# Optimization experiments

Measured on AMD Instinct MI355X. Metric: run time of the kernel, lower is better.

Reference implementation:

```python
import jax, jax.numpy as jnp
import numpy as np

N_NODES = 200000
N_GRAPHS = 64
K_SLOTS = 16
LATENT = 128
HID = 128  # hidden_dim // 2


def setup_inputs() -> dict:
    key = jax.random.key(0)
    ks = jax.random.split(key, 8)
    z = jax.random.normal(ks[0], (N_GRAPHS, K_SLOTS, LATENT), dtype=jnp.float32)
    s = jax.random.uniform(ks[1], (N_NODES, K_SLOTS), dtype=jnp.float32)
    batch = jnp.sort(jax.random.randint(ks[2], (N_NODES,), 0, N_GRAPHS))
    sc1 = 1.0 / np.sqrt(LATENT)
    sc2 = 1.0 / np.sqrt(HID)
    W1 = jax.random.normal(ks[3], (LATENT, HID), dtype=jnp.float32) * sc1
    b1 = jnp.zeros((HID,), dtype=jnp.float32)
    W2 = jax.random.normal(ks[4], (HID, HID), dtype=jnp.float32) * sc2
    b2 = jnp.zeros((HID,), dtype=jnp.float32)
    Wp = jax.random.normal(ks[5], (HID, 2), dtype=jnp.float32) * sc2
    bp = jnp.zeros((2,), dtype=jnp.float32)
    Wv = jax.random.normal(ks[6], (HID, 2), dtype=jnp.float32) * sc2
    bv = jnp.zeros((2,), dtype=jnp.float32)
    return {"z": z, "s": s, "batch": batch, "W1": W1, "b1": b1,
            "W2": W2, "b2": b2, "Wp": Wp, "bp": bp, "Wv": Wv, "bv": bv}


def reference(z, s, batch, W1, b1, W2, b2, Wp, bp, Wv, bv):
    # gather per-node latent set: [N, K, D]
    z_expanded = z[batch]
    # weighted sum over K slots -> [N, D]
    node_feat = jnp.einsum('nk,nkd->nd', s, z_expanded)
    # shared MLP: Linear-ReLU-Linear-ReLU
    h = jax.nn.relu(node_feat @ W1 + b1)
    h = jax.nn.relu(h @ W2 + b2)
    # heads
    pos_recon = jnp.tanh(h @ Wp + bp)
    vel_recon = h @ Wv + bv
    return jnp.concatenate([pos_recon, vel_recon], axis=-1)
```

## Files before the change

kernel.cpp:

```cpp
#include <hip/hip_runtime.h>

typedef _Float16 half4 __attribute__((ext_vector_type(4)));
typedef float    f32x4 __attribute__((ext_vector_type(4)));

#define MFMA16(a,b,c) __builtin_amdgcn_mfma_f32_16x16x16f16((a),(b),(c),0,0,0)

static constexpr int N_NODES  = 200000;
static constexpr int N_GRAPHS = 64;
static constexpr int GPG      = 256;
static constexpr int TOTAL_G  = N_GRAPHS * GPG;

static constexpr size_t WS_ZWT    = 0;
static constexpr size_t WS_W2T    = 262144;
static constexpr size_t WS_WHT    = 294912;
static constexpr size_t WS_GSTART = 299008;

__global__ __launch_bounds__(256) void gnn_prep(
    const int* __restrict__ batch,
    const float* __restrict__ z,
    const float* __restrict__ W1,
    const float* __restrict__ W2,
    const float* __restrict__ Wp,
    const float* __restrict__ Wv,
    int* __restrict__ gstart,
    _Float16* __restrict__ zwt,
    _Float16* __restrict__ w2t,
    _Float16* __restrict__ wht)
{
    const int b = blockIdx.x, t = threadIdx.x;
    if (b < 782) {
        const int i = b * 256 + t;
        if (i < N_NODES) {
            const int bi   = batch[i];
            const int prev = (i == 0) ? -1 : batch[i - 1];
            if (bi != prev)
                for (int g = prev + 1; g <= bi; ++g) gstart[g] = i;
            if (i == N_NODES - 1)
                for (int g = bi + 1; g <= N_GRAPHS; ++g) gstart[g] = N_NODES;
        }
    } else if (b < 846) {
        const int e = (b - 782) * 256 + t;
        const int n = e >> 7, kk = e & 127;
        w2t[e] = (_Float16)W2[kk * 128 + n];
    } else if (b < 854) {
        const int e = (b - 846) * 256 + t;
        const int j = e >> 7, d = e & 127;
        float v = 0.f;
        if (j < 2)      v = Wp[d * 2 + j];
        else if (j < 4) v = Wv[d * 2 + (j - 2)];
        wht[e] = (_Float16)v;
    } else {
        const int p = (b - 854) * 2 + (t >> 7);
        const int g = p >> 4, k = p & 15, d = t & 127;
        const float* zr = z + (g * 16 + k) * 128;
        float a0 = 0.f, a1 = 0.f, a2 = 0.f, a3 = 0.f;
#pragma unroll 8
        for (int c = 0; c < 128; c += 4) {
            a0 += zr[c    ] * W1[(c    ) * 128 + d];
            a1 += zr[c + 1] * W1[(c + 1) * 128 + d];
            a2 += zr[c + 2] * W1[(c + 2) * 128 + d];
            a3 += zr[c + 3] * W1[(c + 3) * 128 + d];
        }
        zwt[(g * 128 + d) * 16 + k] = (_Float16)((a0 + a1) + (a2 + a3));
    }
}

__device__ inline float fast_tanh(float x) {
    x = fminf(fmaxf(x, -15.f), 15.f);
    const float e = __expf(2.f * x);
    return (e - 1.f) / (e + 1.f);
}

__global__ __launch_bounds__(256, 2) void gnn_main(
    const float* __restrict__ s,
    const float* __restrict__ b1,
    const float* __restrict__ b2,
    const float* __restrict__ bp,
    const float* __restrict__ bv,
    const _Float16* __restrict__ zwt,
    const _Float16* __restrict__ w2t,
    const _Float16* __restrict__ wht,
    const int* __restrict__ gstart,
    float* __restrict__ out)
{
    const int lane = threadIdx.x & 63;
    const int n16  = lane & 15;
    const int quad = lane >> 4;
    const int wid  = blockIdx.x * 4 + (threadIdx.x >> 6);
    const int nw   = gridDim.x * 4;

    half4 a2[8][8];
#pragma unroll
    for (int mt = 0; mt < 8; ++mt)
#pragma unroll
        for (int t = 0; t < 8; ++t)
            a2[mt][t] = *(const half4*)(w2t + (mt * 16 + n16) * 128 + t * 16 + quad * 4);

    half4 a3[8];
#pragma unroll
    for (int t = 0; t < 8; ++t)
        a3[t] = *(const half4*)(wht + n16 * 128 + t * 16 + quad * 4);

    const float bp0 = bp[0], bp1 = bp[1], bv0 = bv[0], bv1 = bv[1];

    for (int gi = wid; gi < TOTAL_G; gi += nw) {
        const int g    = gi >> 8;
        const int idx  = gi & 255;
        const int gs   = gstart[g];
        const int ge   = gstart[g + 1];
        const int base = gs + idx * 16;
        if (base >= ge) continue;

        const int node  = base + n16;
        const bool valid = node < ge;

        half4 bs = {(_Float16)0.f, (_Float16)0.f, (_Float16)0.f, (_Float16)0.f};
        if (valid) {
            const f32x4 sv = *(const f32x4*)(s + node * 16 + quad * 4);
            bs[0] = (_Float16)sv[0]; bs[1] = (_Float16)sv[1];
            bs[2] = (_Float16)sv[2]; bs[3] = (_Float16)sv[3];
        }

        const _Float16* zg = zwt + g * 2048;
        half4 h1[8];
#pragma unroll
        for (int mt = 0; mt < 8; ++mt) {
            const half4 a1 = *(const half4*)(zg + (mt * 16 + n16) * 16 + quad * 4);
            const f32x4 zc = {0.f, 0.f, 0.f, 0.f};
            const f32x4 acc = MFMA16(a1, bs, zc);
            const f32x4 bb = *(const f32x4*)(b1 + mt * 16 + quad * 4);
#pragma unroll
            for (int i = 0; i < 4; ++i)
                h1[mt][i] = (_Float16)fmaxf(acc[i] + bb[i], 0.f);
        }

        f32x4 acc3 = {0.f, 0.f, 0.f, 0.f};
#pragma unroll
        for (int mo = 0; mo < 8; ++mo) {
            f32x4 acc2 = {0.f, 0.f, 0.f, 0.f};
#pragma unroll
            for (int t = 0; t < 8; ++t)
                acc2 = MFMA16(a2[mo][t], h1[t], acc2);
            const f32x4 bb = *(const f32x4*)(b2 + mo * 16 + quad * 4);
            half4 h2;
#pragma unroll
            for (int i = 0; i < 4; ++i)
                h2[i] = (_Float16)fmaxf(acc2[i] + bb[i], 0.f);
            acc3 = MFMA16(a3[mo], h2, acc3);
        }

        if (quad == 0 && valid) {
            f32x4 o;
            o[0] = fast_tanh(acc3[0] + bp0);
            o[1] = fast_tanh(acc3[1] + bp1);
            o[2] = acc3[2] + bv0;
            o[3] = acc3[3] + bv1;
            *(f32x4*)(out + node * 4) = o;
        }
    }
}

extern "C" void kernel_launch(void* const* d_in, const int* in_sizes, int n_in,
                              void* d_out, int out_size, void* d_ws, size_t ws_size,
                              hipStream_t stream)
{
    const float* z     = (const float*)d_in[0];
    const float* s     = (const float*)d_in[1];
    const int*   batch = (const int*)d_in[2];
    const float* W1    = (const float*)d_in[3];
    const float* b1    = (const float*)d_in[4];
    const float* W2    = (const float*)d_in[5];
    const float* b2    = (const float*)d_in[6];
    const float* Wp    = (const float*)d_in[7];
    const float* bp    = (const float*)d_in[8];
    const float* Wv    = (const float*)d_in[9];
    const float* bv    = (const float*)d_in[10];
    float* out = (float*)d_out;

    char* w = (char*)d_ws;
    _Float16* zwt = (_Float16*)(w + WS_ZWT);
    _Float16* w2t = (_Float16*)(w + WS_W2T);
    _Float16* wht = (_Float16*)(w + WS_WHT);
    int* gstart   = (int*)(w + WS_GSTART);

    hipLaunchKernelGGL(gnn_prep, dim3(1366), dim3(256), 0, stream,
                       batch, z, W1, W2, Wp, Wv, gstart, zwt, w2t, wht);
    hipLaunchKernelGGL(gnn_main, dim3(512), dim3(256), 0, stream,
                       s, b1, b2, bp, bv, zwt, w2t, wht, gstart, out);
}
```

Measured before the change: 126.9 us.

## Stage MLP weights in LDS, process two node tiles per wave, raise occupancy

W2 and head weights move out of per-thread registers (64 half4 per lane) into shared memory, packed as half8, with the biases staged there too. This frees registers so launch bounds can go to 4 blocks per SM and the grid doubles to 1024 blocks. Each wave now handles 32 nodes as two 16-node MFMA tiles that share each weight fetch, which amortizes LDS reads. Biases are folded into the MFMA accumulator init. The cost is LDS bandwidth and a prologue copy in every block.

```diff
diff --git a/kernel.cpp b/kernel.cpp
--- a/kernel.cpp
+++ b/kernel.cpp
@@ -1,19 +1,21 @@
 #include <hip/hip_runtime.h>
 
 typedef _Float16 half4 __attribute__((ext_vector_type(4)));
+typedef _Float16 half8 __attribute__((ext_vector_type(8)));
 typedef float    f32x4 __attribute__((ext_vector_type(4)));
 
 #define MFMA16(a,b,c) __builtin_amdgcn_mfma_f32_16x16x16f16((a),(b),(c),0,0,0)
 
 static constexpr int N_NODES  = 200000;
 static constexpr int N_GRAPHS = 64;
-static constexpr int GPG      = 256;
-static constexpr int TOTAL_G  = N_GRAPHS * GPG;
+static constexpr int SGPG     = 128;
+static constexpr int TOTAL_SG = N_GRAPHS * SGPG;
 
 static constexpr size_t WS_ZWT    = 0;
 static constexpr size_t WS_W2T    = 262144;
 static constexpr size_t WS_WHT    = 294912;
 static constexpr size_t WS_GSTART = 299008;
+
 
 __global__ __launch_bounds__(256) void gnn_prep(
     const int* __restrict__ batch,
@@ -71,7 +73,7 @@
     return (e - 1.f) / (e + 1.f);
 }
 
-__global__ __launch_bounds__(256, 2) void gnn_main(
+__global__ __launch_bounds__(256, 4) void gnn_main(
     const float* __restrict__ s,
     const float* __restrict__ b1,
     const float* __restrict__ b2,
@@ -83,79 +85,129 @@
     const int* __restrict__ gstart,
     float* __restrict__ out)
 {
-    const int lane = threadIdx.x & 63;
+    __shared__ char lds[37888];
+    half8* a2l = (half8*)lds;
+    half4* a3l = (half4*)(lds + 32768);
+    float* b1l = (float*)(lds + 36864);
+    float* b2l = (float*)(lds + 37376);
+
+    const int tid  = threadIdx.x;
+    const int lane = tid & 63;
     const int n16  = lane & 15;
     const int quad = lane >> 4;
-    const int wid  = blockIdx.x * 4 + (threadIdx.x >> 6);
-    const int nw   = gridDim.x * 4;
-
-    half4 a2[8][8];
-#pragma unroll
-    for (int mt = 0; mt < 8; ++mt)
-#pragma unroll
-        for (int t = 0; t < 8; ++t)
-            a2[mt][t] = *(const half4*)(w2t + (mt * 16 + n16) * 128 + t * 16 + quad * 4);
-
-    half4 a3[8];
-#pragma unroll
-    for (int t = 0; t < 8; ++t)
-        a3[t] = *(const half4*)(wht + n16 * 128 + t * 16 + quad * 4);
+
+#pragma unroll
+    for (int r = 0; r < 8; ++r) {
+        const int e  = r * 256 + tid;
+        const int mo = e >> 8, tp = (e >> 6) & 3, ll = e & 63;
+        const int nn = ll & 15, qq = ll >> 4;
+        const _Float16* srcp = w2t + (mo * 16 + nn) * 128 + tp * 32 + qq * 4;
+        half8 v;
+        *(half4*)&v     = *(const half4*)srcp;
+        *((half4*)&v+1) = *(const half4*)(srcp + 16);
+        a2l[e] = v;
+    }
+    {
+        const int e = tid;
+#pragma unroll
+        for (int r = 0; r < 2; ++r) {
+            const int ee = r * 256 + e;
+            const int tt = ee >> 6, ll = ee & 63;
+            const int nn = ll & 15, qq = ll >> 4;
+            a3l[ee] = *(const half4*)(wht + nn * 128 + tt * 16 + qq * 4);
+        }
+        if (tid < 128)      b1l[tid] = b1[tid];
+        else                b2l[tid - 128] = b2[tid - 128];
+    }
+    __syncthreads();
 
     const float bp0 = bp[0], bp1 = bp[1], bv0 = bv[0], bv1 = bv[1];
-
-    for (int gi = wid; gi < TOTAL_G; gi += nw) {
-        const int g    = gi >> 8;
-        const int idx  = gi & 255;
+    f32x4 c3init = {0.f, 0.f, 0.f, 0.f};
+    if (quad == 0) { c3init[0] = bp0; c3init[1] = bp1; c3init[2] = bv0; c3init[3] = bv1; }
+
+    const int wid = blockIdx.x * 4 + (tid >> 6);
+    const int nw  = gridDim.x * 4;
+
+    for (int sgi = wid; sgi < TOTAL_SG; sgi += nw) {
+        const int g    = sgi >> 7;
+        const int idx  = sgi & 127;
         const int gs   = gstart[g];
         const int ge   = gstart[g + 1];
-        const int base = gs + idx * 16;
+        const int base = gs + idx * 32;
         if (base >= ge) continue;
 
-        const int node  = base + n16;
-        const bool valid = node < ge;
-
-        half4 bs = {(_Float16)0.f, (_Float16)0.f, (_Float16)0.f, (_Float16)0.f};
-        if (valid) {
-            const f32x4 sv = *(const f32x4*)(s + node * 16 + quad * 4);
-            bs[0] = (_Float16)sv[0]; bs[1] = (_Float16)sv[1];
-            bs[2] = (_Float16)sv[2]; bs[3] = (_Float16)sv[3];
+        const int nodeA = base + n16;
+        const int nodeB = base + 16 + n16;
+        const bool vA = nodeA < ge;
+        const bool vB = nodeB < ge;
+
+        half4 bsA = {(_Float16)0.f, (_Float16)0.f, (_Float16)0.f, (_Float16)0.f};
+        half4 bsB = bsA;
+        if (vA) {
+            const f32x4 sv = *(const f32x4*)(s + nodeA * 16 + quad * 4);
+            bsA[0] = (_Float16)sv[0]; bsA[1] = (_Float16)sv[1];
+            bsA[2] = (_Float16)sv[2]; bsA[3] = (_Float16)sv[3];
+        }
+        if (vB) {
+            const f32x4 sv = *(const f32x4*)(s + nodeB * 16 + quad * 4);
+            bsB[0] = (_Float16)sv[0]; bsB[1] = (_Float16)sv[1];
+            bsB[2] = (_Float16)sv[2]; bsB[3] = (_Float16)sv[3];
         }
 
         const _Float16* zg = zwt + g * 2048;
-        half4 h1[8];
+        half4 h1a[8], h1b[8];
 #pragma unroll
         for (int mt = 0; mt < 8; ++mt) {
             const half4 a1 = *(const half4*)(zg + (mt * 16 + n16) * 16 + quad * 4);
-            const f32x4 zc = {0.f, 0.f, 0.f, 0.f};
-            const f32x4 acc = MFMA16(a1, bs, zc);
-            const f32x4 bb = *(const f32x4*)(b1 + mt * 16 + quad * 4);
-#pragma unroll
-            for (int i = 0; i < 4; ++i)
-                h1[mt][i] = (_Float16)fmaxf(acc[i] + bb[i], 0.f);
-        }
-
-        f32x4 acc3 = {0.f, 0.f, 0.f, 0.f};
+            const f32x4 cb = *(const f32x4*)(b1l + mt * 16 + quad * 4);
+            const f32x4 accA = MFMA16(a1, bsA, cb);
+            const f32x4 accB = MFMA16(a1, bsB, cb);
+#pragma unroll
+            for (int i = 0; i < 4; ++i) {
+                h1a[mt][i] = (_Float16)fmaxf(accA[i], 0.f);
+                h1b[mt][i] = (_Float16)fmaxf(accB[i], 0.f);
+            }
+        }
+
+        f32x4 acc3a = c3init, acc3b = c3init;
 #pragma unroll
         for (int mo = 0; mo < 8; ++mo) {
-            f32x4 acc2 = {0.f, 0.f, 0.f, 0.f};
-#pragma unroll
-            for (int t = 0; t < 8; ++t)
-                acc2 = MFMA16(a2[mo][t], h1[t], acc2);
-            const f32x4 bb = *(const f32x4*)(b2 + mo * 16 + quad * 4);
-            half4 h2;
-#pragma unroll
-            for (int i = 0; i < 4; ++i)
-                h2[i] = (_Float16)fmaxf(acc2[i] + bb[i], 0.f);
-            acc3 = MFMA16(a3[mo], h2, acc3);
-        }
-
-        if (quad == 0 && valid) {
-            f32x4 o;
-            o[0] = fast_tanh(acc3[0] + bp0);
-            o[1] = fast_tanh(acc3[1] + bp1);
-            o[2] = acc3[2] + bv0;
-            o[3] = acc3[3] + bv1;
-            *(f32x4*)(out + node * 4) = o;
+            const f32x4 cb = *(const f32x4*)(b2l + mo * 16 + quad * 4);
+            f32x4 a2a = cb, a2b = cb;
+#pragma unroll
+            for (int tp = 0; tp < 4; ++tp) {
+                const half8 w = a2l[(mo * 4 + tp) * 64 + lane];
+                const half4 wlo = {w[0], w[1], w[2], w[3]};
+                const half4 whi = {w[4], w[5], w[6], w[7]};
+                a2a = MFMA16(wlo, h1a[tp * 2], a2a);
+                a2a = MFMA16(whi, h1a[tp * 2 + 1], a2a);
+                a2b = MFMA16(wlo, h1b[tp * 2], a2b);
+                a2b = MFMA16(whi, h1b[tp * 2 + 1], a2b);
+            }
+            half4 h2a, h2b;
+#pragma unroll
+            for (int i = 0; i < 4; ++i) {
+                h2a[i] = (_Float16)fmaxf(a2a[i], 0.f);
+                h2b[i] = (_Float16)fmaxf(a2b[i], 0.f);
+            }
+            const half4 w3 = a3l[mo * 64 + lane];
+            acc3a = MFMA16(w3, h2a, acc3a);
+            acc3b = MFMA16(w3, h2b, acc3b);
+        }
+
+        if (quad == 0) {
+            if (vA) {
+                f32x4 o;
+                o[0] = fast_tanh(acc3a[0]); o[1] = fast_tanh(acc3a[1]);
+                o[2] = acc3a[2];            o[3] = acc3a[3];
+                *(f32x4*)(out + nodeA * 4) = o;
+            }
+            if (vB) {
+                f32x4 o;
+                o[0] = fast_tanh(acc3b[0]); o[1] = fast_tanh(acc3b[1]);
+                o[2] = acc3b[2];            o[3] = acc3b[3];
+                *(f32x4*)(out + nodeB * 4) = o;
+            }
         }
     }
 }
@@ -185,6 +237,6 @@
 
     hipLaunchKernelGGL(gnn_prep, dim3(1366), dim3(256), 0, stream,
                        batch, z, W1, W2, Wp, Wv, gstart, zwt, w2t, wht);
-    hipLaunchKernelGGL(gnn_main, dim3(512), dim3(256), 0, stream,
+    hipLaunchKernelGGL(gnn_main, dim3(1024), dim3(256), 0, stream,
                        s, b1, b2, bp, bv, zwt, w2t, wht, gstart, out);
 }
```

Result: faster. 113.7 us (-10.4%).
